# Kernel optimization log

Hardware: AMD Instinct MI355X
Metric: run time of the kernel (lower is better)

The kernel has to match this reference:

```python
import jax, jax.numpy as jnp
import numpy as np
import math

NUM_HEADS = 16
HEAD_DIM = 64
EMBED = NUM_HEADS * HEAD_DIM  # 1024
T_FEAT = 128


def setup_inputs() -> dict:
    key = jax.random.key(0)
    ks = jax.random.split(key, 9)
    B, S = 4, 2048
    x = jax.random.normal(ks[0], (B, S, EMBED), dtype=jnp.float32)
    time_enc = jax.random.normal(ks[1], (B, T_FEAT), dtype=jnp.float32)
    s = 1.0 / math.sqrt(EMBED)
    Wq = jax.random.normal(ks[2], (EMBED, EMBED), dtype=jnp.float32) * s
    Wk = jax.random.normal(ks[3], (EMBED, EMBED), dtype=jnp.float32) * s
    Wv = jax.random.normal(ks[4], (EMBED, EMBED), dtype=jnp.float32) * s
    Wo = jax.random.normal(ks[5], (EMBED, EMBED), dtype=jnp.float32) * s
    bo = jnp.zeros((EMBED,), dtype=jnp.float32)
    Wt = jax.random.normal(ks[6], (T_FEAT, NUM_HEADS), dtype=jnp.float32) * (1.0 / math.sqrt(T_FEAT))
    bt = jnp.zeros((NUM_HEADS,), dtype=jnp.float32)
    return {"x": x, "time_enc": time_enc, "Wq": Wq, "Wk": Wk, "Wv": Wv,
            "Wo": Wo, "bo": bo, "Wt": Wt, "bt": bt}


def reference(x, time_enc, Wq, Wk, Wv, Wo, bo, Wt, bt):
    B, S, E = x.shape
    H, D = NUM_HEADS, HEAD_DIM
    scale = 1.0 / math.sqrt(D)
    # projections (no bias on q/k/v, bias on out)
    q = (x @ Wq).reshape(B, S, H, D).transpose(0, 2, 1, 3)  # [B,H,S,D]
    k = (x @ Wk).reshape(B, S, H, D).transpose(0, 2, 1, 3)
    v = (x @ Wv).reshape(B, S, H, D).transpose(0, 2, 1, 3)
    scores = jnp.einsum('bhqd,bhkd->bhqk', q, k) * scale
    # time-dependent per-head weighting (softmax over heads)
    time_weights = jax.nn.softmax(time_enc @ Wt + bt)  # [B,H]
    scores = scores * time_weights.reshape(B, H, 1, 1)
    attn = jax.nn.softmax(scores, axis=-1)
    out = jnp.einsum('bhqk,bhkd->bhqd', attn, v)
    out = out.transpose(0, 2, 1, 3).reshape(B, S, E)
    return out @ Wo + bo
```

## Files before the change

kernel.cpp:

```cpp
#include <hip/hip_runtime.h>
#include <cstdint>
#include <cstddef>

#define EMB   1024
#define NH    16
#define HD    64
#define SEQ   2048
#define NB    4
#define MROWS 8192

typedef short short8 __attribute__((ext_vector_type(8)));
typedef float floatx4 __attribute__((ext_vector_type(4)));

__device__ __forceinline__ unsigned short f2bf(float f) {
  return (unsigned short)((__float_as_uint(f) + 0x8000u) >> 16);
}

__device__ __forceinline__ void load16_lds(const unsigned short* g, unsigned short* l) {
  __builtin_amdgcn_global_load_lds((const __attribute__((address_space(1))) void*)g,
                                   (__attribute__((address_space(3))) void*)l, 16, 0, 0);
}

__global__ void time_weights_kernel(const float* __restrict__ te, const float* __restrict__ Wt,
                                    const float* __restrict__ bt, float* __restrict__ tw) {
  int t = threadIdx.x;
  int b = t >> 4, h = t & 15;
  float acc = bt[h];
  for (int i = 0; i < 128; i++) acc += te[b * 128 + i] * Wt[i * 16 + h];
  float m = acc;
  for (int off = 1; off < 16; off <<= 1) m = fmaxf(m, __shfl_xor(m, off, 16));
  float e = __expf(acc - m);
  float s = e;
  for (int off = 1; off < 16; off <<= 1) s += __shfl_xor(s, off, 16);
  tw[t] = (e / s) * 0.125f * 1.4426950408889634f;
}

__global__ void convert_x_kernel(const float4* __restrict__ x, unsigned short* __restrict__ out) {
  int i = blockIdx.x * blockDim.x + threadIdx.x;
  float4 v = x[i];
  unsigned int u0 = __float_as_uint(v.x) + 0x8000u, u1 = __float_as_uint(v.y) + 0x8000u;
  unsigned int u2 = __float_as_uint(v.z) + 0x8000u, u3 = __float_as_uint(v.w) + 0x8000u;
  uint2 p;
  p.x = (u0 >> 16) | (u1 & 0xffff0000u);
  p.y = (u2 >> 16) | (u3 & 0xffff0000u);
  *(uint2*)&out[(size_t)i * 4] = p;
}

__global__ void transpose_convert4_kernel(const float* __restrict__ Wq, const float* __restrict__ Wk,
                                          const float* __restrict__ Wv, const float* __restrict__ Wo,
                                          unsigned short* __restrict__ wqkvt, unsigned short* __restrict__ wot) {
  __shared__ float tile[32][33];
  int z = blockIdx.z;
  const float* W = (z == 0) ? Wq : (z == 1) ? Wk : (z == 2) ? Wv : Wo;
  unsigned short* out = (z < 3) ? (wqkvt + (size_t)z * EMB * EMB) : wot;
  int k0 = blockIdx.x * 32;
  int n0 = blockIdx.y * 32;
  int tx = threadIdx.x;
  int ty = threadIdx.y;
#pragma unroll
  for (int i = 0; i < 4; i++) {
    int k = ty + i * 8;
    tile[k][tx] = W[(size_t)(k0 + k) * EMB + n0 + tx];
  }
  __syncthreads();
#pragma unroll
  for (int i = 0; i < 4; i++) {
    int n = ty + i * 8;
    out[(size_t)(n0 + n) * EMB + k0 + tx] = f2bf(tile[tx][n]);
  }
}

template <int EPI>
__global__ __launch_bounds__(512, 2) void gemm_kernel(
    const unsigned short* __restrict__ A, const unsigned short* __restrict__ Bt,
    unsigned short* __restrict__ qo, unsigned short* __restrict__ ko, unsigned short* __restrict__ vto,
    float* __restrict__ outf, const float* __restrict__ bias, const float* __restrict__ tw) {
  __shared__ unsigned short ldsu[32768];

  const int tid = threadIdx.x;
  const int lane = tid & 63, wid = tid >> 6;
  const int quad = lane >> 4, l16 = lane & 15;
  const int wm = wid >> 2, wn = wid & 3;

  const int gx = gridDim.x;
  const int nwg = gx * gridDim.y;
  const int fid = blockIdx.y * gx + blockIdx.x;
  const int swzid = (fid & 7) * (nwg >> 3) + (fid >> 3);
  const int m0 = (swzid / gx) * 256;
  const int n0 = (swzid % gx) * 256;

  const int trow = tid >> 2;
  const int sw = (((tid & 3) ^ ((tid >> 2) & 3) ^ ((tid >> 4) & 3))) * 8;
  const unsigned short* gA0 = A + (size_t)(m0 + trow) * 1024 + sw;
  const unsigned short* gA1 = A + (size_t)(m0 + 128 + trow) * 1024 + sw;
  const unsigned short* gB0 = Bt + (size_t)(n0 + trow) * 1024 + sw;
  const unsigned short* gB1 = Bt + (size_t)(n0 + 128 + trow) * 1024 + sw;
  unsigned short* lds_w = ldsu + (wid << 9);

  const int swl = (l16 & 3) ^ (l16 >> 2);
  const int foff = (quad ^ swl) * 8;
  const int abase = (wm * 128 + l16) * 32 + foff;
  const int bbase = 8192 + (wn * 64 + l16) * 32 + foff;

  floatx4 acc[8][4];
#pragma unroll
  for (int mi = 0; mi < 8; mi++)
#pragma unroll
    for (int ni = 0; ni < 4; ni++)
#pragma unroll
      for (int r = 0; r < 4; r++) acc[mi][ni][r] = 0.f;

  load16_lds(gA0, lds_w);
  load16_lds(gA1, lds_w + 4096);
  load16_lds(gB0, lds_w + 8192);
  load16_lds(gB1, lds_w + 12288);

  for (int t = 0; t < 32; ++t) {
    const int cur = (t & 1) << 14;
    const int nxt = ((t + 1) & 1) << 14;
    const int kc = ((t + 1) & 31) * 32;
    load16_lds(gA0 + kc, lds_w + nxt);
    load16_lds(gA1 + kc, lds_w + nxt + 4096);
    load16_lds(gB0 + kc, lds_w + nxt + 8192);
    load16_lds(gB1 + kc, lds_w + nxt + 12288);
    asm volatile("s_waitcnt vmcnt(4)" ::: "memory");
    asm volatile("s_barrier" ::: "memory");

    short8 af[8], bf[4];
#pragma unroll
    for (int mi = 0; mi < 8; mi++) af[mi] = *(const short8*)&ldsu[cur + abase + mi * 512];
#pragma unroll
    for (int ni = 0; ni < 4; ni++) bf[ni] = *(const short8*)&ldsu[cur + bbase + ni * 512];
    __builtin_amdgcn_s_setprio(1);
#pragma unroll
    for (int mi = 0; mi < 8; mi++)
#pragma unroll
      for (int ni = 0; ni < 4; ni++)
        acc[mi][ni] = __builtin_amdgcn_mfma_f32_16x16x32_bf16(af[mi], bf[ni], acc[mi][ni], 0, 0, 0);
    __builtin_amdgcn_s_setprio(0);
    asm volatile("s_barrier" ::: "memory");
  }
  asm volatile("s_waitcnt vmcnt(0)" ::: "memory");

  if (EPI == 1) {
#pragma unroll
    for (int mi = 0; mi < 8; mi++)
#pragma unroll
      for (int ni = 0; ni < 4; ni++) {
        const int n = n0 + wn * 64 + ni * 16 + l16;
        const float bs = bias[n];
        const int mb = m0 + wm * 128 + mi * 16 + quad * 4;
#pragma unroll
        for (int r = 0; r < 4; r++)
          outf[(size_t)(mb + r) * EMB + n] = acc[mi][ni][r] + bs;
      }
  } else {
    const int proj = n0 >> 10;
    const int b = m0 >> 11;
    const int hw = ((n0 + wn * 64) >> 6) & 15;
    const size_t bh = (size_t)b * NH + hw;
    const int mbase = m0 + wm * 128;
    if (proj == 0) {
      const float tws = tw[bh];
#pragma unroll
      for (int mi = 0; mi < 8; mi++) {
        const int s = ((mbase + mi * 16) & 2047) + quad * 4;
#pragma unroll
        for (int ni = 0; ni < 4; ni++) {
          const int d = ni * 16 + l16;
          unsigned short* qp = qo + (bh * SEQ + s) * HD + d;
#pragma unroll
          for (int r = 0; r < 4; r++) qp[(size_t)r * HD] = f2bf(acc[mi][ni][r] * tws);
        }
      }
    } else if (proj == 1) {
#pragma unroll
      for (int mi = 0; mi < 8; mi++) {
        const int s = ((mbase + mi * 16) & 2047) + quad * 4;
#pragma unroll
        for (int ni = 0; ni < 4; ni++) {
          const int d = ni * 16 + l16;
          unsigned short* kp = ko + (bh * SEQ + s) * HD + d;
#pragma unroll
          for (int r = 0; r < 4; r++) kp[(size_t)r * HD] = f2bf(acc[mi][ni][r]);
        }
      }
    } else {
#pragma unroll
      for (int mi = 0; mi < 8; mi++) {
        const int s = ((mbase + mi * 16) & 2047) + quad * 4;
#pragma unroll
        for (int ni = 0; ni < 4; ni++) {
          const int d = ni * 16 + l16;
          unsigned int u0 = __float_as_uint(acc[mi][ni][0]) + 0x8000u;
          unsigned int u1 = __float_as_uint(acc[mi][ni][1]) + 0x8000u;
          unsigned int u2 = __float_as_uint(acc[mi][ni][2]) + 0x8000u;
          unsigned int u3 = __float_as_uint(acc[mi][ni][3]) + 0x8000u;
          uint2 w;
          w.x = (u0 >> 16) | (u1 & 0xffff0000u);
          w.y = (u2 >> 16) | (u3 & 0xffff0000u);
          *(uint2*)&vto[(bh * HD + d) * SEQ + s] = w;
        }
      }
    }
  }
}

__global__ __launch_bounds__(256, 4) void attn_kernel(
    const unsigned short* __restrict__ qg, const unsigned short* __restrict__ kg,
    const unsigned short* __restrict__ vtg, unsigned short* __restrict__ aog) {
  __shared__ unsigned short Ks[64 * 64];
  __shared__ unsigned short Vs[64 * 64];
  __shared__ unsigned short Ps[4 * 2048];

  int tid = threadIdx.x;
  int lane = tid & 63, wid = tid >> 6;
  int quad = lane >> 4, l16 = lane & 15, l7 = lane & 7;
  int qt = blockIdx.x, h = blockIdx.y, b = blockIdx.z;
  int bh = b * NH + h;
  const unsigned short* qbase = qg + (size_t)bh * SEQ * HD + (size_t)qt * 128 * HD;
  const unsigned short* kbase = kg + (size_t)bh * SEQ * HD;
  const unsigned short* vbase = vtg + (size_t)bh * HD * SEQ;

  short8 b_q[2][2];
#pragma unroll
  for (int mi = 0; mi < 2; mi++)
#pragma unroll
    for (int kk = 0; kk < 2; kk++)
      b_q[mi][kk] = *(const short8*)&qbase[(wid * 32 + mi * 16 + l16) * 64 + kk * 32 + quad * 8];

  const unsigned short* gK[2];
  const unsigned short* gV[2];
  unsigned short* lK[2];
  unsigned short* lV[2];
#pragma unroll
  for (int c = 0; c < 2; c++) {
    int row = wid * 16 + c * 8 + (lane >> 3);
    int gcol = ((lane & 7) ^ (row & 7)) * 8;
    gK[c] = kbase + row * 64 + gcol;
    gV[c] = vbase + (size_t)row * SEQ + gcol;
    lK[c] = &Ks[(wid * 16 + c * 8) * 64];
    lV[c] = &Vs[(wid * 16 + c * 8) * 64];
  }

  int pg[2];
#pragma unroll
  for (int i = 0; i < 2; i++) pg[i] = l16 * 64 + (((i * 4 + quad) ^ l7) * 8);

  int wbase = wid * 2048;
  int chunkx = l16 & 14;
  int pwa[4];
#pragma unroll
  for (int ni = 0; ni < 4; ni++)
    pwa[ni] = wbase + l16 * 64 + (((ni * 4 + quad) ^ chunkx) * 4);
  int pra[2];
#pragma unroll
  for (int kk2 = 0; kk2 < 2; kk2++)
    pra[kk2] = wbase + l16 * 64 + (((kk2 * 8 + quad * 2) ^ chunkx) * 4);

  floatx4 O[4][2];
  float lsum[2] = {0.f, 0.f};
#pragma unroll
  for (int di = 0; di < 4; di++)
#pragma unroll
    for (int mi = 0; mi < 2; mi++)
#pragma unroll
      for (int r = 0; r < 4; r++) O[di][mi][r] = 0.f;

  for (int kb = 0; kb < 32; kb++) {
    __syncthreads();
#pragma unroll
    for (int c = 0; c < 2; c++) {
      load16_lds(gK[c] + kb * 4096, lK[c]);
      load16_lds(gV[c] + kb * 64, lV[c]);
    }
    asm volatile("s_waitcnt vmcnt(0) lgkmcnt(0)" ::: "memory");
    __syncthreads();

    floatx4 st[4][2];
#pragma unroll
    for (int ni = 0; ni < 4; ni++)
#pragma unroll
      for (int mi = 0; mi < 2; mi++)
#pragma unroll
        for (int r = 0; r < 4; r++) st[ni][mi][r] = 0.f;
#pragma unroll
    for (int kk = 0; kk < 2; kk++)
#pragma unroll
      for (int ni = 0; ni < 4; ni++) {
        short8 a_k = *(const short8*)&Ks[ni * 1024 + pg[kk]];
#pragma unroll
        for (int mi = 0; mi < 2; mi++)
          st[ni][mi] = __builtin_amdgcn_mfma_f32_16x16x32_bf16(a_k, b_q[mi][kk], st[ni][mi], 0, 0, 0);
      }

#pragma unroll
    for (int mi = 0; mi < 2; mi++)
#pragma unroll
      for (int ni = 0; ni < 4; ni++) {
        float p0 = __builtin_amdgcn_exp2f(st[ni][mi][0]);
        float p1 = __builtin_amdgcn_exp2f(st[ni][mi][1]);
        float p2 = __builtin_amdgcn_exp2f(st[ni][mi][2]);
        float p3 = __builtin_amdgcn_exp2f(st[ni][mi][3]);
        lsum[mi] += (p0 + p1) + (p2 + p3);
        unsigned int u0 = __float_as_uint(p0) + 0x8000u, u1 = __float_as_uint(p1) + 0x8000u;
        unsigned int u2 = __float_as_uint(p2) + 0x8000u, u3 = __float_as_uint(p3) + 0x8000u;
        uint2 w;
        w.x = (u0 >> 16) | (u1 & 0xffff0000u);
        w.y = (u2 >> 16) | (u3 & 0xffff0000u);
        *(uint2*)&Ps[pwa[ni] + mi * 1024] = w;
      }
    asm volatile("s_waitcnt lgkmcnt(0)" ::: "memory");

#pragma unroll
    for (int kk2 = 0; kk2 < 2; kk2++) {
      short8 av[4], bp[2];
#pragma unroll
      for (int di = 0; di < 4; di++)
        av[di] = *(const short8*)&Vs[di * 1024 + pg[kk2]];
#pragma unroll
      for (int mi = 0; mi < 2; mi++)
        bp[mi] = *(const short8*)&Ps[pra[kk2] + mi * 1024];
#pragma unroll
      for (int di = 0; di < 4; di++)
#pragma unroll
        for (int mi = 0; mi < 2; mi++)
          O[di][mi] = __builtin_amdgcn_mfma_f32_16x16x32_bf16(av[di], bp[mi], O[di][mi], 0, 0, 0);
    }
  }

  float inv[2];
#pragma unroll
  for (int mi = 0; mi < 2; mi++) {
    lsum[mi] += __shfl_xor(lsum[mi], 16);
    lsum[mi] += __shfl_xor(lsum[mi], 32);
    inv[mi] = 1.0f / lsum[mi];
  }

#pragma unroll
  for (int mi = 0; mi < 2; mi++) {
    int s = qt * 128 + wid * 32 + mi * 16 + l16;
    size_t rowbase = ((size_t)(b * SEQ + s) * NH + h) * HD;
#pragma unroll
    for (int di = 0; di < 4; di++) {
      unsigned int u0 = __float_as_uint(O[di][mi][0] * inv[mi]) + 0x8000u;
      unsigned int u1 = __float_as_uint(O[di][mi][1] * inv[mi]) + 0x8000u;
      unsigned int u2 = __float_as_uint(O[di][mi][2] * inv[mi]) + 0x8000u;
      unsigned int u3 = __float_as_uint(O[di][mi][3] * inv[mi]) + 0x8000u;
      uint2 w;
      w.x = (u0 >> 16) | (u1 & 0xffff0000u);
      w.y = (u2 >> 16) | (u3 & 0xffff0000u);
      *(uint2*)&aog[rowbase + di * 16 + quad * 4] = w;
    }
  }
}

extern "C" void kernel_launch(void* const* d_in, const int* in_sizes, int n_in,
                              void* d_out, int out_size, void* d_ws, size_t ws_size,
                              hipStream_t stream) {
  (void)in_sizes; (void)n_in; (void)out_size; (void)ws_size;
  const float* x  = (const float*)d_in[0];
  const float* te = (const float*)d_in[1];
  const float* Wq = (const float*)d_in[2];
  const float* Wk = (const float*)d_in[3];
  const float* Wv = (const float*)d_in[4];
  const float* Wo = (const float*)d_in[5];
  const float* bo = (const float*)d_in[6];
  const float* Wt = (const float*)d_in[7];
  const float* bt = (const float*)d_in[8];
  float* out = (float*)d_out;

  char* ws = (char*)d_ws;
  size_t off = 0;
  auto carve = [&](size_t bytes) -> void* {
    void* p = ws + off;
    off += (bytes + 255) & ~(size_t)255;
    return p;
  };
  float* twb            = (float*)carve(64 * sizeof(float));
  unsigned short* xb    = (unsigned short*)carve((size_t)MROWS * EMB * 2);
  unsigned short* wqkvt = (unsigned short*)carve((size_t)3 * EMB * EMB * 2);
  unsigned short* wot   = (unsigned short*)carve((size_t)EMB * EMB * 2);
  unsigned short* vtb   = (unsigned short*)carve((size_t)MROWS * EMB * 2);
  unsigned short* qb    = (unsigned short*)d_out;
  unsigned short* kb    = (unsigned short*)d_out + (size_t)MROWS * EMB;
  unsigned short* ao    = xb;

  time_weights_kernel<<<dim3(1), dim3(64), 0, stream>>>(te, Wt, bt, twb);
  convert_x_kernel<<<dim3(8192), dim3(256), 0, stream>>>((const float4*)x, xb);
  transpose_convert4_kernel<<<dim3(32, 32, 4), dim3(32, 8), 0, stream>>>(Wq, Wk, Wv, Wo, wqkvt, wot);
  gemm_kernel<0><<<dim3(12, 32), dim3(512), 0, stream>>>(xb, wqkvt, qb, kb, vtb, nullptr, nullptr, twb);
  attn_kernel<<<dim3(16, NH, NB), dim3(256), 0, stream>>>(qb, kb, vtb, ao);
  gemm_kernel<1><<<dim3(4, 32), dim3(512), 0, stream>>>(ao, wot, nullptr, nullptr, nullptr, out, bo, nullptr);
}
```

Measured before the change: 302.3 us.

## Restructure GEMM to 128x256 tiles with 4 waves and interleaved load/MFMA phases

The projection GEMMs move from 256x256 tiles with 8 waves to 128x256 tiles with 4 waves, which doubles the grid and shrinks the LDS buffers. The K loop is split into four sub-phases: each phase issues part of the next tile's global-to-LDS loads, reads fragments and runs a quarter of the MFMAs. The aim is to overlap memory traffic with compute and improve CU fill. The price is more barriers per iteration, fragile hand-written waitcnt counts, and lower arithmetic intensity per block.

```diff
diff --git a/kernel.cpp b/kernel.cpp
--- a/kernel.cpp
+++ b/kernel.cpp
@@ -71,36 +71,33 @@
 }
 
 template <int EPI>
-__global__ __launch_bounds__(512, 2) void gemm_kernel(
+__global__ __launch_bounds__(256, 2) void gemm_kernel(
     const unsigned short* __restrict__ A, const unsigned short* __restrict__ Bt,
     unsigned short* __restrict__ qo, unsigned short* __restrict__ ko, unsigned short* __restrict__ vto,
     float* __restrict__ outf, const float* __restrict__ bias, const float* __restrict__ tw) {
-  __shared__ unsigned short ldsu[32768];
+  __shared__ unsigned short ldsu[24576];
 
   const int tid = threadIdx.x;
   const int lane = tid & 63, wid = tid >> 6;
   const int quad = lane >> 4, l16 = lane & 15;
-  const int wm = wid >> 2, wn = wid & 3;
 
   const int gx = gridDim.x;
   const int nwg = gx * gridDim.y;
   const int fid = blockIdx.y * gx + blockIdx.x;
   const int swzid = (fid & 7) * (nwg >> 3) + (fid >> 3);
-  const int m0 = (swzid / gx) * 256;
+  const int m0 = (swzid / gx) * 128;
   const int n0 = (swzid % gx) * 256;
 
   const int trow = tid >> 2;
-  const int sw = (((tid & 3) ^ ((tid >> 2) & 3) ^ ((tid >> 4) & 3))) * 8;
-  const unsigned short* gA0 = A + (size_t)(m0 + trow) * 1024 + sw;
-  const unsigned short* gA1 = A + (size_t)(m0 + 128 + trow) * 1024 + sw;
-  const unsigned short* gB0 = Bt + (size_t)(n0 + trow) * 1024 + sw;
-  const unsigned short* gB1 = Bt + (size_t)(n0 + 128 + trow) * 1024 + sw;
-  unsigned short* lds_w = ldsu + (wid << 9);
+  const int sw = ((tid & 3) ^ ((tid >> 2) & 3) ^ ((tid >> 4) & 3)) * 8;
+  const unsigned short* gA = A + (size_t)(m0 + trow) * 1024 + sw;
+  const unsigned short* gB = Bt + (size_t)(n0 + trow) * 1024 + sw;
+  unsigned short* lw = ldsu + (wid << 9);
 
   const int swl = (l16 & 3) ^ (l16 >> 2);
   const int foff = (quad ^ swl) * 8;
-  const int abase = (wm * 128 + l16) * 32 + foff;
-  const int bbase = 8192 + (wn * 64 + l16) * 32 + foff;
+  const int abase = l16 * 32 + foff;
+  const int bbase = 4096 + wid * 1024 + l16 * 32 + foff;
 
   floatx4 acc[8][4];
 #pragma unroll
@@ -110,64 +107,114 @@
 #pragma unroll
       for (int r = 0; r < 4; r++) acc[mi][ni][r] = 0.f;
 
-  load16_lds(gA0, lds_w);
-  load16_lds(gA1, lds_w + 4096);
-  load16_lds(gB0, lds_w + 8192);
-  load16_lds(gB1, lds_w + 12288);
-
+  load16_lds(gB, lw + 4096);
+  load16_lds(gB + 65536, lw + 6144);
+  load16_lds(gA, lw);
+  load16_lds(gB + 131072, lw + 8192);
+  load16_lds(gB + 196608, lw + 10240);
+  load16_lds(gA + 65536, lw + 2048);
+  asm volatile("s_waitcnt vmcnt(3)" ::: "memory");
+  asm volatile("s_barrier" ::: "memory");
+
+  short8 aF[4], b0F[2], b1F[2];
   for (int t = 0; t < 32; ++t) {
-    const int cur = (t & 1) << 14;
-    const int nxt = ((t + 1) & 1) << 14;
+    const int cur = (t & 1) ? 12288 : 0;
+    const int nxt = (t & 1) ? 0 : 12288;
     const int kc = ((t + 1) & 31) * 32;
-    load16_lds(gA0 + kc, lds_w + nxt);
-    load16_lds(gA1 + kc, lds_w + nxt + 4096);
-    load16_lds(gB0 + kc, lds_w + nxt + 8192);
-    load16_lds(gB1 + kc, lds_w + nxt + 12288);
+
+#pragma unroll
+    for (int mi = 0; mi < 4; mi++) aF[mi] = *(const short8*)&ldsu[cur + abase + mi * 512];
+#pragma unroll
+    for (int ni = 0; ni < 2; ni++) b0F[ni] = *(const short8*)&ldsu[cur + bbase + ni * 512];
+    load16_lds(gB + kc, lw + nxt + 4096);
+    load16_lds(gB + 65536 + kc, lw + nxt + 6144);
+    asm volatile("s_waitcnt vmcnt(3)" ::: "memory");
+    asm volatile("s_barrier" ::: "memory");
+    asm volatile("s_waitcnt lgkmcnt(0)" ::: "memory");
+    __builtin_amdgcn_sched_barrier(0);
+    __builtin_amdgcn_s_setprio(1);
+#pragma unroll
+    for (int mi = 0; mi < 4; mi++)
+#pragma unroll
+      for (int ni = 0; ni < 2; ni++)
+        acc[mi][ni] = __builtin_amdgcn_mfma_f32_16x16x32_bf16(aF[mi], b0F[ni], acc[mi][ni], 0, 0, 0);
+    __builtin_amdgcn_s_setprio(0);
+    asm volatile("s_barrier" ::: "memory");
+
+#pragma unroll
+    for (int ni = 0; ni < 2; ni++) b1F[ni] = *(const short8*)&ldsu[cur + bbase + 4096 + ni * 512];
+    load16_lds(gA + kc, lw + nxt);
+    load16_lds(gB + 131072 + kc, lw + nxt + 8192);
     asm volatile("s_waitcnt vmcnt(4)" ::: "memory");
     asm volatile("s_barrier" ::: "memory");
-
-    short8 af[8], bf[4];
-#pragma unroll
-    for (int mi = 0; mi < 8; mi++) af[mi] = *(const short8*)&ldsu[cur + abase + mi * 512];
-#pragma unroll
-    for (int ni = 0; ni < 4; ni++) bf[ni] = *(const short8*)&ldsu[cur + bbase + ni * 512];
+    asm volatile("s_waitcnt lgkmcnt(0)" ::: "memory");
+    __builtin_amdgcn_sched_barrier(0);
     __builtin_amdgcn_s_setprio(1);
 #pragma unroll
-    for (int mi = 0; mi < 8; mi++)
-#pragma unroll
-      for (int ni = 0; ni < 4; ni++)
-        acc[mi][ni] = __builtin_amdgcn_mfma_f32_16x16x32_bf16(af[mi], bf[ni], acc[mi][ni], 0, 0, 0);
+    for (int mi = 0; mi < 4; mi++)
+#pragma unroll
+      for (int ni = 0; ni < 2; ni++)
+        acc[mi][2 + ni] = __builtin_amdgcn_mfma_f32_16x16x32_bf16(aF[mi], b1F[ni], acc[mi][2 + ni], 0, 0, 0);
     __builtin_amdgcn_s_setprio(0);
     asm volatile("s_barrier" ::: "memory");
+
+#pragma unroll
+    for (int mi = 0; mi < 4; mi++) aF[mi] = *(const short8*)&ldsu[cur + abase + 2048 + mi * 512];
+    load16_lds(gB + 196608 + kc, lw + nxt + 10240);
+    asm volatile("s_barrier" ::: "memory");
+    asm volatile("s_waitcnt lgkmcnt(0)" ::: "memory");
+    __builtin_amdgcn_sched_barrier(0);
+    __builtin_amdgcn_s_setprio(1);
+#pragma unroll
+    for (int mi = 0; mi < 4; mi++)
+#pragma unroll
+      for (int ni = 0; ni < 2; ni++)
+        acc[4 + mi][2 + ni] = __builtin_amdgcn_mfma_f32_16x16x32_bf16(aF[mi], b1F[ni], acc[4 + mi][2 + ni], 0, 0, 0);
+    __builtin_amdgcn_s_setprio(0);
+    asm volatile("s_barrier" ::: "memory");
+
+    load16_lds(gA + 65536 + kc, lw + nxt + 2048);
+    asm volatile("s_waitcnt vmcnt(3)" ::: "memory");
+    asm volatile("s_barrier" ::: "memory");
+    __builtin_amdgcn_s_setprio(1);
+#pragma unroll
+    for (int mi = 0; mi < 4; mi++)
+#pragma unroll
+      for (int ni = 0; ni < 2; ni++)
+        acc[4 + mi][ni] = __builtin_amdgcn_mfma_f32_16x16x32_bf16(aF[mi], b0F[ni], acc[4 + mi][ni], 0, 0, 0);
+    __builtin_amdgcn_s_setprio(0);
+    asm volatile("s_barrier" ::: "memory");
   }
   asm volatile("s_waitcnt vmcnt(0)" ::: "memory");
 
   if (EPI == 1) {
 #pragma unroll
-    for (int mi = 0; mi < 8; mi++)
-#pragma unroll
-      for (int ni = 0; ni < 4; ni++) {
-        const int n = n0 + wn * 64 + ni * 16 + l16;
-        const float bs = bias[n];
-        const int mb = m0 + wm * 128 + mi * 16 + quad * 4;
+    for (int ni = 0; ni < 4; ni++) {
+      const int n = n0 + (ni >> 1) * 128 + wid * 32 + (ni & 1) * 16 + l16;
+      const float bs = bias[n];
+#pragma unroll
+      for (int mi = 0; mi < 8; mi++) {
+        const int mb = m0 + mi * 16 + quad * 4;
 #pragma unroll
         for (int r = 0; r < 4; r++)
           outf[(size_t)(mb + r) * EMB + n] = acc[mi][ni][r] + bs;
       }
+    }
   } else {
     const int proj = n0 >> 10;
     const int b = m0 >> 11;
-    const int hw = ((n0 + wn * 64) >> 6) & 15;
-    const size_t bh = (size_t)b * NH + hw;
-    const int mbase = m0 + wm * 128;
+    const int sb = (m0 & 2047) + quad * 4;
     if (proj == 0) {
-      const float tws = tw[bh];
-#pragma unroll
-      for (int mi = 0; mi < 8; mi++) {
-        const int s = ((mbase + mi * 16) & 2047) + quad * 4;
-#pragma unroll
-        for (int ni = 0; ni < 4; ni++) {
-          const int d = ni * 16 + l16;
+#pragma unroll
+      for (int ni = 0; ni < 4; ni++) {
+        const int nb = n0 + (ni >> 1) * 128 + wid * 32 + (ni & 1) * 16;
+        const int hh = (nb >> 6) & 15;
+        const int d = (nb & 63) + l16;
+        const size_t bh = (size_t)b * NH + hh;
+        const float tws = tw[bh];
+#pragma unroll
+        for (int mi = 0; mi < 8; mi++) {
+          const int s = sb + mi * 16;
           unsigned short* qp = qo + (bh * SEQ + s) * HD + d;
 #pragma unroll
           for (int r = 0; r < 4; r++) qp[(size_t)r * HD] = f2bf(acc[mi][ni][r] * tws);
@@ -175,11 +222,14 @@
       }
     } else if (proj == 1) {
 #pragma unroll
-      for (int mi = 0; mi < 8; mi++) {
-        const int s = ((mbase + mi * 16) & 2047) + quad * 4;
-#pragma unroll
-        for (int ni = 0; ni < 4; ni++) {
-          const int d = ni * 16 + l16;
+      for (int ni = 0; ni < 4; ni++) {
+        const int nb = n0 + (ni >> 1) * 128 + wid * 32 + (ni & 1) * 16;
+        const int hh = (nb >> 6) & 15;
+        const int d = (nb & 63) + l16;
+        const size_t bh = (size_t)b * NH + hh;
+#pragma unroll
+        for (int mi = 0; mi < 8; mi++) {
+          const int s = sb + mi * 16;
           unsigned short* kp = ko + (bh * SEQ + s) * HD + d;
 #pragma unroll
           for (int r = 0; r < 4; r++) kp[(size_t)r * HD] = f2bf(acc[mi][ni][r]);
@@ -187,11 +237,14 @@
       }
     } else {
 #pragma unroll
-      for (int mi = 0; mi < 8; mi++) {
-        const int s = ((mbase + mi * 16) & 2047) + quad * 4;
-#pragma unroll
-        for (int ni = 0; ni < 4; ni++) {
-          const int d = ni * 16 + l16;
+      for (int ni = 0; ni < 4; ni++) {
+        const int nb = n0 + (ni >> 1) * 128 + wid * 32 + (ni & 1) * 16;
+        const int hh = (nb >> 6) & 15;
+        const int d = (nb & 63) + l16;
+        const size_t bh = (size_t)b * NH + hh;
+#pragma unroll
+        for (int mi = 0; mi < 8; mi++) {
+          const int s = sb + mi * 16;
           unsigned int u0 = __float_as_uint(acc[mi][ni][0]) + 0x8000u;
           unsigned int u1 = __float_as_uint(acc[mi][ni][1]) + 0x8000u;
           unsigned int u2 = __float_as_uint(acc[mi][ni][2]) + 0x8000u;
@@ -389,7 +442,7 @@
   time_weights_kernel<<<dim3(1), dim3(64), 0, stream>>>(te, Wt, bt, twb);
   convert_x_kernel<<<dim3(8192), dim3(256), 0, stream>>>((const float4*)x, xb);
   transpose_convert4_kernel<<<dim3(32, 32, 4), dim3(32, 8), 0, stream>>>(Wq, Wk, Wv, Wo, wqkvt, wot);
-  gemm_kernel<0><<<dim3(12, 32), dim3(512), 0, stream>>>(xb, wqkvt, qb, kb, vtb, nullptr, nullptr, twb);
+  gemm_kernel<0><<<dim3(12, 64), dim3(256), 0, stream>>>(xb, wqkvt, qb, kb, vtb, nullptr, nullptr, twb);
   attn_kernel<<<dim3(16, NH, NB), dim3(256), 0, stream>>>(qb, kb, vtb, ao);
-  gemm_kernel<1><<<dim3(4, 32), dim3(512), 0, stream>>>(ao, wot, nullptr, nullptr, nullptr, out, bo, nullptr);
-}
+  gemm_kernel<1><<<dim3(4, 64), dim3(256), 0, stream>>>(ao, wot, nullptr, nullptr, nullptr, out, bo, nullptr);
+}
```

After: 292.3 us. -3.3%, faster.
